# Optimization experiments

Measured on AMD Instinct MI355X. Metric: run time of the kernel, lower is better.

## Reference

```python
import jax, jax.numpy as jnp
import numpy as np

L = 2048      # seq_len
E = 2048      # hidden_dim
H = 16        # num_heads
D = E // H    # head_dim


def setup_inputs() -> dict:
    key = jax.random.key(0)
    ks = jax.random.split(key, 6)
    x = jax.random.normal(ks[0], (L, E), dtype=jnp.float32)
    bias_matrix = jax.random.normal(ks[1], (L, L), dtype=jnp.float32) * 0.1
    # nn.MultiheadAttention params: packed in_proj [3E, E] + bias [3E], out_proj [E, E] + bias [E]
    in_proj_weight = jax.random.normal(ks[2], (3 * E, E), dtype=jnp.float32) * 0.02
    in_proj_bias = jax.random.normal(ks[3], (3 * E,), dtype=jnp.float32) * 0.02
    out_proj_weight = jax.random.normal(ks[4], (E, E), dtype=jnp.float32) * 0.02
    out_proj_bias = jax.random.normal(ks[5], (E,), dtype=jnp.float32) * 0.02
    return {
        "x": x,
        "bias_matrix": bias_matrix,
        "in_proj_weight": in_proj_weight,
        "in_proj_bias": in_proj_bias,
        "out_proj_weight": out_proj_weight,
        "out_proj_bias": out_proj_bias,
    }


def reference(x, bias_matrix, in_proj_weight, in_proj_bias, out_proj_weight, out_proj_bias):
    # Packed QKV projection (torch Linear convention: y = x @ W.T + b)
    qkv = x @ in_proj_weight.T + in_proj_bias            # [L, 3E]
    q, k, v = jnp.split(qkv, 3, axis=-1)                 # each [L, E]
    q = q.reshape(L, H, D)
    k = k.reshape(L, H, D)
    v = v.reshape(L, H, D)
    scale = 1.0 / jnp.sqrt(jnp.asarray(D, dtype=x.dtype))
    # scores: [H, L, L]; bias_matrix broadcast over heads (torch 2D attn_mask semantics)
    scores = jnp.einsum("lhd,mhd->hlm", q * scale, k) + bias_matrix[None, :, :]
    attn = jax.nn.softmax(scores, axis=-1)
    ctx = jnp.einsum("hlm,mhd->lhd", attn, v).reshape(L, E)
    out = ctx @ out_proj_weight.T + out_proj_bias        # [L, E]
    return out
```

## Files before the change

kernel.cpp:

```cpp
#include <hip/hip_runtime.h>
#include <math.h>

#define L_SEQ 2048
#define E_DIM 2048
#define H_NUM 16
#define D_HEAD 128

typedef __attribute__((ext_vector_type(8))) _Float16 half8;
typedef __attribute__((ext_vector_type(4))) _Float16 half4;
typedef __attribute__((ext_vector_type(4))) float floatx4;

static __device__ __forceinline__ void gload16(const void* g, void* lds) {
  __builtin_amdgcn_global_load_lds(
      (const __attribute__((address_space(1))) void*)g,
      (__attribute__((address_space(3))) void*)lds, 16, 0, 0);
}

__global__ __launch_bounds__(256)
void cvt3_f32_f16(const float* __restrict__ a, _Float16* __restrict__ oa, int na,
                  const float* __restrict__ b, _Float16* __restrict__ ob, int nb,
                  const float* __restrict__ c, _Float16* __restrict__ oc, int nc) {
  int i = (blockIdx.x * 256 + threadIdx.x) * 8;
  const float* src;
  _Float16* dst;
  if (i < na) {
    src = a + i; dst = oa + i;
  } else if (i < na + nb) {
    src = b + (i - na); dst = ob + (i - na);
  } else if (i < na + nb + nc) {
    src = c + (i - na - nb); dst = oc + (i - na - nb);
  } else {
    return;
  }
  float4 p = *(const float4*)src;
  float4 q = *(const float4*)(src + 4);
  half8 h = {(_Float16)p.x, (_Float16)p.y, (_Float16)p.z, (_Float16)p.w,
             (_Float16)q.x, (_Float16)q.y, (_Float16)q.z, (_Float16)q.w};
  *(half8*)dst = h;
}

template <int TM, int TN, int WR, int WC, int EPI>
__global__ __launch_bounds__(256)
void gemm_mfma(const _Float16* __restrict__ A, const _Float16* __restrict__ B,
               const float* __restrict__ bias, float* __restrict__ C,
               _Float16* __restrict__ qk, _Float16* __restrict__ vt,
               int M, int N, int K) {
  constexpr int RT = TM / (16 * WR);
  constexpr int CT = TN / (16 * WC);
  constexpr int ACH = TM / 8;
  constexpr int NCH = (TM + TN) / 32;

  __shared__ _Float16 As[2][TM * 64];
  __shared__ _Float16 Bs[2][TN * 64];

  const int tid = threadIdx.x;
  const int wave = tid >> 6, lane = tid & 63;
  const int l15 = lane & 15, quad = lane >> 4;
  const int wr = wave / WC, wc = wave % WC;
  const int row0 = blockIdx.y * TM, col0 = blockIdx.x * TN;

  const int srow = lane >> 3;
  const int gc = (lane & 7) ^ srow;

  auto stage = [&](int buf, int k0) {
#pragma unroll
    for (int c = 0; c < NCH; ++c) {
      int chunk = wave * NCH + c;
      if (chunk < ACH) {
        int row = chunk * 8 + srow;
        gload16((const char*)(A + (size_t)(row0 + row) * K + k0) + gc * 16,
                (char*)&As[buf][0] + chunk * 1024);
      } else {
        int bch = chunk - ACH;
        int row = bch * 8 + srow;
        gload16((const char*)(B + (size_t)(col0 + row) * K + k0) + gc * 16,
                (char*)&Bs[buf][0] + bch * 1024);
      }
    }
  };

  floatx4 acc[RT][CT];
#pragma unroll
  for (int i = 0; i < RT; ++i)
#pragma unroll
    for (int j = 0; j < CT; ++j) acc[i][j] = (floatx4){0.f, 0.f, 0.f, 0.f};

  const int niter = K / 64;
  stage(0, 0);

  for (int it = 0; it < niter; ++it) {
    const int cur = it & 1;
    __syncthreads();
    if (it + 1 < niter) stage(cur ^ 1, (it + 1) * 64);

#pragma unroll
    for (int ks = 0; ks < 2; ++ks) {
      half8 af[RT], bf[CT];
#pragma unroll
      for (int t = 0; t < RT; ++t) {
        int r = wr * (16 * RT) + t * 16 + l15;
        af[t] = *(const half8*)&As[cur][r * 64 + (((ks * 4 + quad) ^ (r & 7)) * 8)];
      }
#pragma unroll
      for (int t = 0; t < CT; ++t) {
        int r = wc * (16 * CT) + t * 16 + l15;
        bf[t] = *(const half8*)&Bs[cur][r * 64 + (((ks * 4 + quad) ^ (r & 7)) * 8)];
      }
#pragma unroll
      for (int tr = 0; tr < RT; ++tr)
#pragma unroll
        for (int tc = 0; tc < CT; ++tc)
          acc[tr][tc] = __builtin_amdgcn_mfma_f32_16x16x32_f16(
              af[tr], bf[tc], acc[tr][tc], 0, 0, 0);
    }
  }

  const int crow = row0 + wr * (16 * RT);
  const int ccol = col0 + wc * (16 * CT);

  if (EPI == 0) {
#pragma unroll
    for (int tc = 0; tc < CT; ++tc) {
      int col = ccol + tc * 16 + l15;
      float bb = bias[col];
#pragma unroll
      for (int tr = 0; tr < RT; ++tr)
#pragma unroll
        for (int r = 0; r < 4; ++r)
          C[(size_t)(crow + tr * 16 + quad * 4 + r) * N + col] =
              acc[tr][tc][r] + bb;
    }
  } else if (col0 < 2 * E_DIM) {
#pragma unroll
    for (int tc = 0; tc < CT; ++tc) {
      int col = ccol + tc * 16 + l15;
      float bb = bias[col];
#pragma unroll
      for (int tr = 0; tr < RT; ++tr)
#pragma unroll
        for (int r = 0; r < 4; ++r)
          qk[(size_t)(crow + tr * 16 + quad * 4 + r) * (2 * E_DIM) + col] =
              (_Float16)(acc[tr][tc][r] + bb);
    }
  } else {
#pragma unroll
    for (int tc = 0; tc < CT; ++tc) {
      int col = ccol + tc * 16 + l15;
      float bb = bias[col];
      int vrow = col - 2 * E_DIM;
#pragma unroll
      for (int tr = 0; tr < RT; ++tr) {
        int rbase = crow + tr * 16 + quad * 4;
        half4 h = {(_Float16)(acc[tr][tc][0] + bb), (_Float16)(acc[tr][tc][1] + bb),
                   (_Float16)(acc[tr][tc][2] + bb), (_Float16)(acc[tr][tc][3] + bb)};
        *(half4*)&vt[(size_t)vrow * L_SEQ + rbase] = h;
      }
    }
  }
}

__global__ __launch_bounds__(512, 2)
void attn_mfma(const _Float16* __restrict__ qk, const _Float16* __restrict__ vt,
               const float* __restrict__ bias, _Float16* __restrict__ ctx) {
  const int h = blockIdx.x;
  const int q0 = blockIdx.y * 128;
  const int tid = threadIdx.x;
  const int wave = tid >> 6;
  const int lane = tid & 63;
  const int l15 = lane & 15;
  const int quad = lane >> 4;
  const int g = wave >> 1;
  const int p = wave & 1;

  __shared__ __align__(16) char smem[131072];
  char* const ksmem = smem;
  char* const vsmem = smem + 65536;

  const int qrow = q0 + g * 32;

  half8 qa[2][4];
#pragma unroll
  for (int u = 0; u < 2; ++u) {
    const _Float16* qp =
        qk + (size_t)(qrow + u * 16 + l15) * (2 * E_DIM) + h * D_HEAD + quad * 8;
#pragma unroll
    for (int ks = 0; ks < 4; ++ks) qa[u][ks] = *(const half8*)(qp + ks * 32);
  }

  float l_acc[2] = {0.f, 0.f};
  floatx4 o[2][8];
#pragma unroll
  for (int u = 0; u < 2; ++u)
#pragma unroll
    for (int t = 0; t < 8; ++t) o[u][t] = (floatx4){0.f, 0.f, 0.f, 0.f};

  const float scale = 0.088388347648318447f;

  auto stage_pair = [&](int kt2, int sb) {
#pragma unroll
    for (int c = 0; c < 8; ++c) {
      int mb = c * 512 + (tid & ~63);
      int m = mb + (tid & 63);
      if (mb < 2048) {
        int sub = mb >> 10;
        int idx = m & 1023, idx0 = mb & 1023;
        int row = idx >> 4, cc = idx & 15;
        gload16(qk + (size_t)(kt2 + sub * 64 + row) * (2 * E_DIM) + E_DIM +
                    h * D_HEAD + ((cc ^ (row & 7)) * 8),
                ksmem + (sb + sub) * 16384 + idx0 * 16);
      } else {
        int mm = mb - 2048;
        int sub = mm >> 10;
        int idx = (m - 2048) & 1023, idx0 = mm & 1023;
        int row = idx >> 3, cc = idx & 7;
        gload16(vt + (size_t)(h * D_HEAD + row) * L_SEQ + kt2 + sub * 64 +
                    ((cc ^ (row & 7)) * 8),
                vsmem + (sb + sub) * 16384 + idx0 * 16);
      }
    }
  };

  stage_pair(0, 0);

#pragma unroll 2
  for (int s = 0; s < 16; ++s) {
    const int kt = s * 128 + p * 64;
    const int slot = (s & 1) * 2 + p;
    __syncthreads();

    floatx4 bq[2][4];
#pragma unroll
    for (int u = 0; u < 2; ++u)
#pragma unroll
      for (int t4 = 0; t4 < 4; ++t4)
        bq[u][t4] = *(const floatx4*)&bias[(size_t)(qrow + u * 16 + l15) * L_SEQ +
                                           kt + t4 * 16 + quad * 4];

    if (s < 15) stage_pair((s + 1) * 128, ((s + 1) & 1) * 2);

    const char* ksb = ksmem + slot * 16384;
    floatx4 st[2][4];
#pragma unroll
    for (int u = 0; u < 2; ++u)
#pragma unroll
      for (int t4 = 0; t4 < 4; ++t4) st[u][t4] = (floatx4){0.f, 0.f, 0.f, 0.f};
#pragma unroll
    for (int ks = 0; ks < 4; ++ks)
#pragma unroll
      for (int t4 = 0; t4 < 4; ++t4) {
        int row = t4 * 16 + l15;
        half8 kf = *(const half8*)(ksb + row * 256 +
                                   (((4 * ks + quad) ^ (row & 7)) * 16));
        st[0][t4] = __builtin_amdgcn_mfma_f32_16x16x32_f16(kf, qa[0][ks],
                                                           st[0][t4], 0, 0, 0);
        st[1][t4] = __builtin_amdgcn_mfma_f32_16x16x32_f16(kf, qa[1][ks],
                                                           st[1][t4], 0, 0, 0);
      }

    half4 hp[2][4];
#pragma unroll
    for (int u = 0; u < 2; ++u) {
      float ls = 0.f;
#pragma unroll
      for (int t4 = 0; t4 < 4; ++t4) {
        float p0 = __expf(fmaf(st[u][t4][0], scale, bq[u][t4][0]));
        float p1 = __expf(fmaf(st[u][t4][1], scale, bq[u][t4][1]));
        float p2 = __expf(fmaf(st[u][t4][2], scale, bq[u][t4][2]));
        float p3 = __expf(fmaf(st[u][t4][3], scale, bq[u][t4][3]));
        ls += (p0 + p1) + (p2 + p3);
        hp[u][t4] = (half4){(_Float16)p0, (_Float16)p1, (_Float16)p2, (_Float16)p3};
      }
      ls += __shfl_xor(ls, 16);
      ls += __shfl_xor(ls, 32);
      l_acc[u] += ls;
    }

    const char* vsb = vsmem + slot * 16384;
#pragma unroll
    for (int tk = 0; tk < 4; ++tk)
#pragma unroll
      for (int td = 0; td < 8; ++td) {
        int row = td * 16 + l15;
        half4 vf = *(const half4*)(vsb + row * 128 +
                                   (((2 * tk + (quad >> 1)) ^ (row & 7)) * 16) +
                                   (quad & 1) * 8);
        o[0][td] = __builtin_amdgcn_mfma_f32_16x16x16f16(hp[0][tk], vf,
                                                         o[0][td], 0, 0, 0);
        o[1][td] = __builtin_amdgcn_mfma_f32_16x16x16f16(hp[1][tk], vf,
                                                         o[1][td], 0, 0, 0);
      }
  }

  float* obuf = (float*)smem;
  float* lbuf = (float*)(smem + 73728);
  __syncthreads();
  if (p == 1) {
#pragma unroll
    for (int u = 0; u < 2; ++u)
#pragma unroll
      for (int t = 0; t < 8; ++t)
        *(floatx4*)&obuf[(size_t)(g * 128 + t * 16 + l15) * 36 + u * 16 + quad * 4] =
            o[u][t];
    if (quad == 0) {
      lbuf[(g * 2 + 0) * 16 + l15] = l_acc[0];
      lbuf[(g * 2 + 1) * 16 + l15] = l_acc[1];
    }
  }
  __syncthreads();
  if (p == 0) {
#pragma unroll
    for (int u = 0; u < 2; ++u) {
      float lt = l_acc[u] + lbuf[(g * 2 + u) * 16 + l15];
      float inv[4];
#pragma unroll
      for (int r = 0; r < 4; ++r) inv[r] = 1.f / __shfl(lt, quad * 4 + r);
#pragma unroll
      for (int t = 0; t < 8; ++t) {
        floatx4 part = *(const floatx4*)&obuf[(size_t)(g * 128 + t * 16 + l15) * 36 +
                                              u * 16 + quad * 4];
#pragma unroll
        for (int r = 0; r < 4; ++r) {
          int rowq = qrow + u * 16 + quad * 4 + r;
          ctx[(size_t)rowq * E_DIM + h * D_HEAD + t * 16 + l15] =
              (_Float16)((o[u][t][r] + part[r]) * inv[r]);
        }
      }
    }
  }
}

extern "C" void kernel_launch(void* const* d_in, const int* in_sizes, int n_in,
                              void* d_out, int out_size, void* d_ws, size_t ws_size,
                              hipStream_t stream) {
  const float* x          = (const float*)d_in[0];
  const float* bias_mat   = (const float*)d_in[1];
  const float* in_proj_w  = (const float*)d_in[2];
  const float* in_proj_b  = (const float*)d_in[3];
  const float* out_proj_w = (const float*)d_in[4];
  const float* out_proj_b = (const float*)d_in[5];
  float* out = (float*)d_out;

  _Float16* x16 = (_Float16*)d_ws;
  _Float16* w1  = x16 + (size_t)L_SEQ * E_DIM;
  _Float16* w2  = w1 + (size_t)3 * E_DIM * E_DIM;
  _Float16* qk  = w2 + (size_t)E_DIM * E_DIM;
  _Float16* vt  = qk + (size_t)L_SEQ * 2 * E_DIM;
  _Float16* ctx = vt + (size_t)E_DIM * L_SEQ;

  dim3 blk(256);
  const int nx = L_SEQ * E_DIM, nw1 = 3 * E_DIM * E_DIM, nw2 = E_DIM * E_DIM;

  cvt3_f32_f16<<<(nx + nw1 + nw2) / 2048, blk, 0, stream>>>(
      x, x16, nx, in_proj_w, w1, nw1, out_proj_w, w2, nw2);

  gemm_mfma<128, 128, 2, 2, 1><<<dim3(3 * E_DIM / 128, L_SEQ / 128), blk, 0, stream>>>(
      x16, w1, in_proj_b, nullptr, qk, vt, L_SEQ, 3 * E_DIM, E_DIM);

  attn_mfma<<<dim3(H_NUM, L_SEQ / 128), dim3(512), 0, stream>>>(qk, vt, bias_mat,
                                                                ctx);

  gemm_mfma<128, 64, 4, 1, 0><<<dim3(E_DIM / 64, L_SEQ / 128), blk, 0, stream>>>(
      ctx, w2, out_proj_b, out, nullptr, nullptr, L_SEQ, E_DIM, E_DIM);
}
```

Measured before the change: 282.7 us.

## Split attention key dimension across four waves per query group with 1024-thread blocks

```diff
diff --git a/kernel.cpp b/kernel.cpp
--- a/kernel.cpp
+++ b/kernel.cpp
@@ -159,7 +159,7 @@
   }
 }
 
-__global__ __launch_bounds__(512, 2)
+__global__ __launch_bounds__(1024, 4)
 void attn_mfma(const _Float16* __restrict__ qk, const _Float16* __restrict__ vt,
                const float* __restrict__ bias, _Float16* __restrict__ ctx) {
   const int h = blockIdx.x;
@@ -169,8 +169,8 @@
   const int lane = tid & 63;
   const int l15 = lane & 15;
   const int quad = lane >> 4;
-  const int g = wave >> 1;
-  const int p = wave & 1;
+  const int g = wave >> 2;
+  const int pp = wave & 3;
 
   __shared__ __align__(16) char smem[131072];
   char* const ksmem = smem;
@@ -196,58 +196,50 @@
 
   const float scale = 0.088388347648318447f;
 
-  auto stage_pair = [&](int kt2, int sb) {
-#pragma unroll
-    for (int c = 0; c < 8; ++c) {
-      int mb = c * 512 + (tid & ~63);
+  auto stage_quad = [&](int kt2, int sb) {
+#pragma unroll
+    for (int c = 0; c < 4; ++c) {
+      int mb = c * 1024 + (tid & ~63);
       int m = mb + (tid & 63);
       if (mb < 2048) {
-        int sub = mb >> 10;
-        int idx = m & 1023, idx0 = mb & 1023;
+        int sub = mb >> 9;
+        int idx = m & 511, idx0 = mb & 511;
         int row = idx >> 4, cc = idx & 15;
-        gload16(qk + (size_t)(kt2 + sub * 64 + row) * (2 * E_DIM) + E_DIM +
+        gload16(qk + (size_t)(kt2 + sub * 32 + row) * (2 * E_DIM) + E_DIM +
                     h * D_HEAD + ((cc ^ (row & 7)) * 8),
-                ksmem + (sb + sub) * 16384 + idx0 * 16);
+                ksmem + (sb + sub) * 8192 + idx0 * 16);
       } else {
-        int mm = mb - 2048;
-        int sub = mm >> 10;
-        int idx = (m - 2048) & 1023, idx0 = mm & 1023;
-        int row = idx >> 3, cc = idx & 7;
-        gload16(vt + (size_t)(h * D_HEAD + row) * L_SEQ + kt2 + sub * 64 +
-                    ((cc ^ (row & 7)) * 8),
-                vsmem + (sb + sub) * 16384 + idx0 * 16);
+        int mb2 = mb - 2048;
+        int sub = mb2 >> 9;
+        int idx = (m - 2048) & 511, idx0 = mb2 & 511;
+        int row = idx >> 2, cc = idx & 3;
+        gload16(vt + (size_t)(h * D_HEAD + row) * L_SEQ + kt2 + sub * 32 +
+                    ((cc ^ (row & 3)) * 8),
+                vsmem + (sb + sub) * 8192 + idx0 * 16);
       }
     }
   };
 
-  stage_pair(0, 0);
+  stage_quad(0, 0);
 
 #pragma unroll 2
   for (int s = 0; s < 16; ++s) {
-    const int kt = s * 128 + p * 64;
-    const int slot = (s & 1) * 2 + p;
-    __syncthreads();
-
-    floatx4 bq[2][4];
+    const int kt = s * 128 + pp * 32;
+    const int slot = (s & 1) * 4 + pp;
+    __syncthreads();
+
+    if (s < 15) stage_quad((s + 1) * 128, ((s + 1) & 1) * 4);
+
+    const char* ksb = ksmem + slot * 8192;
+    floatx4 st[2][2];
 #pragma unroll
     for (int u = 0; u < 2; ++u)
 #pragma unroll
-      for (int t4 = 0; t4 < 4; ++t4)
-        bq[u][t4] = *(const floatx4*)&bias[(size_t)(qrow + u * 16 + l15) * L_SEQ +
-                                           kt + t4 * 16 + quad * 4];
-
-    if (s < 15) stage_pair((s + 1) * 128, ((s + 1) & 1) * 2);
-
-    const char* ksb = ksmem + slot * 16384;
-    floatx4 st[2][4];
-#pragma unroll
-    for (int u = 0; u < 2; ++u)
-#pragma unroll
-      for (int t4 = 0; t4 < 4; ++t4) st[u][t4] = (floatx4){0.f, 0.f, 0.f, 0.f};
+      for (int t4 = 0; t4 < 2; ++t4) st[u][t4] = (floatx4){0.f, 0.f, 0.f, 0.f};
 #pragma unroll
     for (int ks = 0; ks < 4; ++ks)
 #pragma unroll
-      for (int t4 = 0; t4 < 4; ++t4) {
+      for (int t4 = 0; t4 < 2; ++t4) {
         int row = t4 * 16 + l15;
         half8 kf = *(const half8*)(ksb + row * 256 +
                                    (((4 * ks + quad) ^ (row & 7)) * 16));
@@ -257,16 +249,18 @@
                                                            st[1][t4], 0, 0, 0);
       }
 
-    half4 hp[2][4];
+    half4 hp[2][2];
 #pragma unroll
     for (int u = 0; u < 2; ++u) {
       float ls = 0.f;
 #pragma unroll
-      for (int t4 = 0; t4 < 4; ++t4) {
-        float p0 = __expf(fmaf(st[u][t4][0], scale, bq[u][t4][0]));
-        float p1 = __expf(fmaf(st[u][t4][1], scale, bq[u][t4][1]));
-        float p2 = __expf(fmaf(st[u][t4][2], scale, bq[u][t4][2]));
-        float p3 = __expf(fmaf(st[u][t4][3], scale, bq[u][t4][3]));
+      for (int t4 = 0; t4 < 2; ++t4) {
+        floatx4 bq = *(const floatx4*)&bias[(size_t)(qrow + u * 16 + l15) * L_SEQ +
+                                            kt + t4 * 16 + quad * 4];
+        float p0 = __expf(fmaf(st[u][t4][0], scale, bq[0]));
+        float p1 = __expf(fmaf(st[u][t4][1], scale, bq[1]));
+        float p2 = __expf(fmaf(st[u][t4][2], scale, bq[2]));
+        float p3 = __expf(fmaf(st[u][t4][3], scale, bq[3]));
         ls += (p0 + p1) + (p2 + p3);
         hp[u][t4] = (half4){(_Float16)p0, (_Float16)p1, (_Float16)p2, (_Float16)p3};
       }
@@ -275,14 +269,14 @@
       l_acc[u] += ls;
     }
 
-    const char* vsb = vsmem + slot * 16384;
-#pragma unroll
-    for (int tk = 0; tk < 4; ++tk)
+    const char* vsb = vsmem + slot * 8192;
+#pragma unroll
+    for (int tk = 0; tk < 2; ++tk)
 #pragma unroll
       for (int td = 0; td < 8; ++td) {
         int row = td * 16 + l15;
-        half4 vf = *(const half4*)(vsb + row * 128 +
-                                   (((2 * tk + (quad >> 1)) ^ (row & 7)) * 16) +
+        half4 vf = *(const half4*)(vsb + row * 64 +
+                                   (((2 * tk + (quad >> 1)) ^ (row & 3)) * 16) +
                                    (quad & 1) * 8);
         o[0][td] = __builtin_amdgcn_mfma_f32_16x16x16f16(hp[0][tk], vf,
                                                          o[0][td], 0, 0, 0);
@@ -292,32 +286,49 @@
   }
 
   float* obuf = (float*)smem;
-  float* lbuf = (float*)(smem + 73728);
+  float* lbuf = (float*)(smem + 81920);
   __syncthreads();
-  if (p == 1) {
-#pragma unroll
-    for (int u = 0; u < 2; ++u)
+  if (quad == 0) {
+    lbuf[((g * 4 + pp) * 2 + 0) * 16 + l15] = l_acc[0];
+    lbuf[((g * 4 + pp) * 2 + 1) * 16 + l15] = l_acc[1];
+  }
+
+#pragma unroll
+  for (int u = 0; u < 2; ++u) {
+    __syncthreads();
+    if (pp >= 2) {
 #pragma unroll
       for (int t = 0; t < 8; ++t)
-        *(floatx4*)&obuf[(size_t)(g * 128 + t * 16 + l15) * 36 + u * 16 + quad * 4] =
-            o[u][t];
-    if (quad == 0) {
-      lbuf[(g * 2 + 0) * 16 + l15] = l_acc[0];
-      lbuf[(g * 2 + 1) * 16 + l15] = l_acc[1];
-    }
-  }
-  __syncthreads();
-  if (p == 0) {
-#pragma unroll
-    for (int u = 0; u < 2; ++u) {
-      float lt = l_acc[u] + lbuf[(g * 2 + u) * 16 + l15];
+        *(floatx4*)&obuf[(size_t)((g * 2 + (pp - 2)) * 128 + t * 16 + l15) * 20 +
+                         quad * 4] = o[u][t];
+    }
+    __syncthreads();
+    if (pp < 2) {
+#pragma unroll
+      for (int t = 0; t < 8; ++t) {
+        floatx4 part = *(const floatx4*)&obuf[(size_t)((g * 2 + pp) * 128 +
+                                                       t * 16 + l15) * 20 + quad * 4];
+        o[u][t] += part;
+      }
+    }
+    __syncthreads();
+    if (pp == 1) {
+#pragma unroll
+      for (int t = 0; t < 8; ++t)
+        *(floatx4*)&obuf[(size_t)(g * 128 + t * 16 + l15) * 20 + quad * 4] = o[u][t];
+    }
+    __syncthreads();
+    if (pp == 0) {
+      float lt = 0.f;
+#pragma unroll
+      for (int j = 0; j < 4; ++j) lt += lbuf[((g * 4 + j) * 2 + u) * 16 + l15];
       float inv[4];
 #pragma unroll
       for (int r = 0; r < 4; ++r) inv[r] = 1.f / __shfl(lt, quad * 4 + r);
 #pragma unroll
       for (int t = 0; t < 8; ++t) {
-        floatx4 part = *(const floatx4*)&obuf[(size_t)(g * 128 + t * 16 + l15) * 36 +
-                                              u * 16 + quad * 4];
+        floatx4 part = *(const floatx4*)&obuf[(size_t)(g * 128 + t * 16 + l15) * 20 +
+                                              quad * 4];
 #pragma unroll
         for (int r = 0; r < 4; ++r) {
           int rowq = qrow + u * 16 + quad * 4 + r;
@@ -356,8 +367,8 @@
   gemm_mfma<128, 128, 2, 2, 1><<<dim3(3 * E_DIM / 128, L_SEQ / 128), blk, 0, stream>>>(
       x16, w1, in_proj_b, nullptr, qk, vt, L_SEQ, 3 * E_DIM, E_DIM);
 
-  attn_mfma<<<dim3(H_NUM, L_SEQ / 128), dim3(512), 0, stream>>>(qk, vt, bias_mat,
-                                                                ctx);
+  attn_mfma<<<dim3(H_NUM, L_SEQ / 128), dim3(1024), 0, stream>>>(qk, vt, bias_mat,
+                                                                 ctx);
 
   gemm_mfma<128, 64, 4, 1, 0><<<dim3(E_DIM / 64, L_SEQ / 128), blk, 0, stream>>>(
       ctx, w2, out_proj_b, out, nullptr, nullptr, L_SEQ, E_DIM, E_DIM);
```

Result: slower. 399.5 us (+41.3%).
